# Kernel tuning notes

Measured on AMD Instinct MI355X. Metric: run time of the kernel, lower is better.

Reference implementation:

```python
import jax, jax.numpy as jnp
import numpy as np

SEQ_LEN, BATCH, VOCAB, EMB, HID, LAYERS = 128, 64, 10000, 1024, 1024, 2

def setup_inputs() -> dict:
    key = jax.random.key(0)
    ks = jax.random.split(key, 8)
    inputs = jax.random.randint(ks[0], (SEQ_LEN, BATCH), 0, VOCAB)
    hidden = jnp.zeros((LAYERS, BATCH, HID), jnp.float32)
    # parameters (uniform init like the torch module)
    emb = jax.random.uniform(ks[1], (VOCAB, EMB), jnp.float32, -0.1, 0.1)
    # per-layer RNN cell params (emb_size == hidden_size so Wx stacks uniformly)
    s = 1.0 / np.sqrt(HID)
    Wx = jax.random.uniform(ks[2], (LAYERS, HID, HID), jnp.float32, -s, s)
    Wh = jax.random.uniform(ks[3], (LAYERS, HID, HID), jnp.float32, -s, s)
    b = jax.random.uniform(ks[4], (LAYERS, HID), jnp.float32, -s, s)
    fcW = jax.random.uniform(ks[5], (VOCAB, HID), jnp.float32, -0.1, 0.1)
    fcb = jnp.zeros((VOCAB,), jnp.float32)
    return {"inputs": inputs, "hidden": hidden, "emb": emb, "Wx": Wx,
            "Wh": Wh, "b": b, "fcW": fcW, "fcb": fcb}

def reference(inputs, hidden, emb, Wx, Wh, b, fcW, fcb):
    num_layers = hidden.shape[0]

    def step(h, tok):
        x = emb[tok]  # [B, EMB] embedding lookup (dropout = identity, keep_prob=1)
        new_h = []
        for j in range(num_layers):  # small static loop over layers
            hj = jnp.tanh(x @ Wx[j] + h[j] @ Wh[j] + b[j])  # [B, H]
            new_h.append(hj)
            x = hj
        logits = x @ fcW.T + fcb  # [B, V]
        return jnp.stack(new_h), logits

    h_final, logits = jax.lax.scan(step, hidden, inputs)
    return logits, h_final  # [S,B,V], [L,B,H]
```

## Files before the change

kernel.cpp:

```cpp
#include <hip/hip_runtime.h>
#include <hip/hip_bf16.h>
#include <math.h>

typedef __hip_bfloat16 bf16;
typedef __attribute__((ext_vector_type(8))) short short8;
typedef __attribute__((ext_vector_type(4))) float floatx4;

#define SEQ   128
#define BATCH 64
#define VOCAB 10000
#define HID   1024
#define TAIL  81920000

#define MFMA(a,b,c) __builtin_amdgcn_mfma_f32_16x16x32_bf16((a),(b),(c),0,0,0)

__device__ inline void gl_lds16(const bf16* g, bf16* s) {
  __builtin_amdgcn_global_load_lds(
      (const __attribute__((address_space(1))) void*)g,
      (__attribute__((address_space(3))) void*)s, 16, 0, 0);
}

__device__ inline float ld_in(const void* p, size_t i, int f) {
  return f ? ((const float*)p)[i] : __bfloat162float(((const bf16*)p)[i]);
}

__global__ __launch_bounds__(256) void detect(const unsigned short* __restrict__ u,
                                              int* __restrict__ flag) {
  __shared__ int smax;
  if (threadIdx.x == 0) smax = 0;
  __syncthreads();
  int mymax = 0;
  for (int i = threadIdx.x * 2; i < 4096; i += 512) {
    int e = (u[i] >> 7) & 0xFF;
    mymax = max(mymax, e);
  }
  atomicMax(&smax, mymax);
  __syncthreads();
  if (threadIdx.x == 0) {
    flag[0] = (smax >= 0xF0) ? 1 : 0;
    flag[1] = 0;
  }
}

__global__ __launch_bounds__(256) void convert_any(const void* __restrict__ src,
                                                   bf16* __restrict__ dst, int n,
                                                   const int* __restrict__ flagp) {
  int f = *flagp;
  for (int i = blockIdx.x * 256 + threadIdx.x; i < n; i += gridDim.x * 256)
    dst[i] = __float2bfloat16(ld_in(src, (size_t)i, f));
}

__global__ __launch_bounds__(256) void transpose4(const void* __restrict__ Wx,
                                                  const void* __restrict__ Wh,
                                                  bf16* __restrict__ Wt,
                                                  const int* __restrict__ flagp) {
  __shared__ bf16 tile[64][65];
  int f = *flagp;
  int z = blockIdx.z;
  const void* src = (z & 1) ? Wh : Wx;
  size_t loff = (z >> 1) ? (size_t)HID * HID : 0;
  bf16* dst = Wt + (size_t)z * HID * HID;
  int r0 = blockIdx.x * 64, c0 = blockIdx.y * 64;
  int t = threadIdx.x, cc = t & 63, rg = t >> 6;
  #pragma unroll
  for (int i = 0; i < 16; ++i) {
    int r = rg * 16 + i;
    tile[r][cc] = __float2bfloat16(ld_in(src, loff + (size_t)(r0 + r) * HID + c0 + cc, f));
  }
  __syncthreads();
  #pragma unroll
  for (int i = 0; i < 16; ++i) {
    int j = rg * 16 + i;
    dst[(size_t)(c0 + j) * HID + r0 + cc] = tile[cc][j];
  }
}

__global__ __launch_bounds__(256) void gemm_a0(
    const int*  __restrict__ tok,
    const bf16* __restrict__ emb,
    const bf16* __restrict__ Wx0t,
    const bf16* __restrict__ b0,
    float* __restrict__ A0)
{
  __shared__ __align__(16) bf16 sA[128 * 32];
  __shared__ __align__(16) bf16 sB[128 * 32];
  int m0 = blockIdx.x * 128, n0 = blockIdx.y * 128;
  int t = threadIdx.x, lane = t & 63, w = t >> 6;
  int wm = (w >> 1) * 64, wn = (w & 1) * 64;
  int quad = lane >> 4, l16 = lane & 15;

  int r0 = t >> 2, kc = t & 3;
  const bf16* ga0 = emb + (size_t)tok[m0 + r0] * HID + kc * 8;
  const bf16* ga1 = emb + (size_t)tok[m0 + r0 + 64] * HID + kc * 8;
  const bf16* gb0 = Wx0t + (size_t)(n0 + r0) * HID + kc * 8;
  const bf16* gb1 = gb0 + (size_t)64 * HID;
  bf16* sa0 = sA + t * 8;  bf16* sa1 = sA + (t + 256) * 8;
  bf16* sb0 = sB + t * 8;  bf16* sb1 = sB + (t + 256) * 8;

  floatx4 acc[4][4];
  #pragma unroll
  for (int j = 0; j < 4; ++j) {
    float bv = __bfloat162float(b0[n0 + wn + j * 16 + l16]);
    #pragma unroll
    for (int i = 0; i < 4; ++i) acc[i][j] = (floatx4){bv, bv, bv, bv};
  }

  for (int kt = 0; kt < 32; ++kt) {
    gl_lds16(ga0, sa0); gl_lds16(ga1, sa1);
    gl_lds16(gb0, sb0); gl_lds16(gb1, sb1);
    ga0 += 32; ga1 += 32; gb0 += 32; gb1 += 32;
    __syncthreads();
    short8 af[4], bfr[4];
    #pragma unroll
    for (int i = 0; i < 4; ++i)
      af[i] = *(const short8*)(sA + (wm + i * 16 + l16) * 32 + quad * 8);
    #pragma unroll
    for (int j = 0; j < 4; ++j)
      bfr[j] = *(const short8*)(sB + (wn + j * 16 + l16) * 32 + quad * 8);
    #pragma unroll
    for (int i = 0; i < 4; ++i)
      #pragma unroll
      for (int j = 0; j < 4; ++j)
        acc[i][j] = MFMA(af[i], bfr[j], acc[i][j]);
    __syncthreads();
  }

  #pragma unroll
  for (int i = 0; i < 4; ++i)
    #pragma unroll
    for (int j = 0; j < 4; ++j)
      #pragma unroll
      for (int r = 0; r < 4; ++r) {
        int row = wm + i * 16 + quad * 4 + r;
        int col = wn + j * 16 + l16;
        A0[(size_t)(m0 + row) * HID + n0 + col] = acc[i][j][r];
      }
}

__device__ inline void gridbar(int* cnt, int expect) {
  __syncthreads();
  if (threadIdx.x == 0) {
    __threadfence();
    __hip_atomic_fetch_add(cnt, 1, __ATOMIC_RELEASE, __HIP_MEMORY_SCOPE_AGENT);
    while (__hip_atomic_load(cnt, __ATOMIC_ACQUIRE, __HIP_MEMORY_SCOPE_AGENT) < expect)
      __builtin_amdgcn_s_sleep(1);
    __threadfence();
  }
  __syncthreads();
}

__global__ __launch_bounds__(256) void wavefront_persist(
    const float* __restrict__ A0,
    const bf16* __restrict__ Wt,
    const bf16* __restrict__ bvecB,
    const bf16* __restrict__ hidB,
    bf16* __restrict__ h0a, bf16* __restrict__ h0b,
    bf16* __restrict__ h1a, bf16* __restrict__ h1b,
    bf16* __restrict__ H1hist,
    void* __restrict__ outv,
    int* __restrict__ flagp)
{
  __shared__ short8 sW8[4096];
  char* sWb = (char*)sW8;
  const int f = flagp[0];
  int* bar = flagp + 1;
  const int blk = blockIdx.x;
  const int t = threadIdx.x, lane = t & 63, w = t >> 6;
  const int quad = lane >> 4, l16 = lane & 15;
  const int m = w * 16;
  const bool isH1 = blk >= 32;

  const bf16* Wh0t = Wt + (size_t)1 * HID * HID;
  const bf16* Wx1t = Wt + (size_t)2 * HID * HID;
  const bf16* Wh1t = Wt + (size_t)3 * HID * HID;

  if (!isH1) {
    const int n0 = blk * 32;
    #pragma unroll
    for (int i = 0; i < 16; ++i) {
      int idx = i * 256 + t;
      int row = idx >> 7, c16 = idx & 127;
      short8 v = *(const short8*)(Wh0t + (size_t)(n0 + row) * HID + c16 * 8);
      int off = (c16 >> 2) * 2048 + (row >> 4) * 1024 + (c16 & 3) * 256 + (row & 15) * 16;
      *(short8*)(sWb + off) = v;
    }
  } else {
    const int n0 = (blk - 32) * 16;
    #pragma unroll
    for (int i = 0; i < 8; ++i) {
      int idx = i * 256 + t;
      int row = idx >> 7, c16 = idx & 127;
      int off = (c16 >> 2) * 1024 + (c16 & 3) * 256 + (row & 15) * 16;
      *(short8*)(sWb + off)         = *(const short8*)(Wx1t + (size_t)(n0 + row) * HID + c16 * 8);
      *(short8*)(sWb + 32768 + off) = *(const short8*)(Wh1t + (size_t)(n0 + row) * HID + c16 * 8);
    }
  }
  __syncthreads();

  for (int k = 0; k <= 128; ++k) {
    if (!isH1) {
      if (k <= 127) {
        const int n0 = blk * 32;
        const bf16* hp = (k == 0) ? hidB : ((k & 1) ? h0a : h0b);
        const bf16* aB = hp + (size_t)(m + l16) * HID + quad * 8;
        const char* b0p = sWb + lane * 16;
        const char* b1p = sWb + 1024 + lane * 16;
        floatx4 acc[2] = {};
        #pragma unroll 8
        for (int kt = 0; kt < 32; ++kt) {
          short8 a = *(const short8*)(aB + kt * 32);
          acc[0] = MFMA(a, *(const short8*)(b0p + kt * 2048), acc[0]);
          acc[1] = MFMA(a, *(const short8*)(b1p + kt * 2048), acc[1]);
        }
        bf16* hw = (k & 1) ? h0b : h0a;
        #pragma unroll
        for (int j = 0; j < 2; ++j)
          #pragma unroll
          for (int r = 0; r < 4; ++r) {
            int row = m + quad * 4 + r, col = n0 + j * 16 + l16;
            float pre = acc[j][r] + A0[(size_t)(k * 64 + row) * HID + col];
            float v = tanhf(pre);
            bf16 bv = __float2bfloat16(v);
            hw[row * HID + col] = bv;
            if (k == 127) {
              size_t o = (size_t)TAIL + row * HID + col;
              if (f) ((float*)outv)[o] = v; else ((bf16*)outv)[o] = bv;
            }
          }
      }
    } else {
      if (k >= 1) {
        const int n0 = (blk - 32) * 16;
        const bf16* a1p = (k & 1) ? h0a : h0b;
        const bf16* a2p = (k == 1) ? (hidB + 64 * HID)
                                   : ((k & 1) ? h1a : h1b);
        const bf16* aB1 = a1p + (size_t)(m + l16) * HID + quad * 8;
        const bf16* aB2 = a2p + (size_t)(m + l16) * HID + quad * 8;
        const char* bXp = sWb + lane * 16;
        const char* bHp = sWb + 32768 + lane * 16;
        floatx4 accX = {}, accH = {};
        #pragma unroll 8
        for (int kt = 0; kt < 32; ++kt) {
          short8 a = *(const short8*)(aB1 + kt * 32);
          accX = MFMA(a, *(const short8*)(bXp + kt * 1024), accX);
          short8 c = *(const short8*)(aB2 + kt * 32);
          accH = MFMA(c, *(const short8*)(bHp + kt * 1024), accH);
        }
        bf16* hw = (k & 1) ? h1b : h1a;
        #pragma unroll
        for (int r = 0; r < 4; ++r) {
          int row = m + quad * 4 + r, col = n0 + l16;
          float v = tanhf(accX[r] + accH[r] + __bfloat162float(bvecB[HID + col]));
          bf16 bv = __float2bfloat16(v);
          hw[row * HID + col] = bv;
          H1hist[(size_t)((k - 1) * 64 + row) * HID + col] = bv;
          if (k == 128) {
            size_t o = (size_t)TAIL + 64 * HID + row * HID + col;
            if (f) ((float*)outv)[o] = v; else ((bf16*)outv)[o] = bv;
          }
        }
      }
    }
    if (k < 128) gridbar(bar, (k + 1) * 96);
  }
}

__global__ __launch_bounds__(256) void gemm_logits(
    const bf16* __restrict__ H1,
    const bf16* __restrict__ fcW,
    const bf16* __restrict__ fcb,
    void* __restrict__ outv,
    const int* __restrict__ flagp)
{
  __shared__ __align__(16) bf16 sA[128 * 32];
  __shared__ __align__(16) bf16 sB[128 * 32];
  int f = *flagp;
  int m0 = blockIdx.x * 128, n0 = blockIdx.y * 128;
  int t = threadIdx.x, lane = t & 63, w = t >> 6;
  int wm = (w >> 1) * 64, wn = (w & 1) * 64;
  int quad = lane >> 4, l16 = lane & 15;

  int r0 = t >> 2, kc = t & 3;
  int rB0 = n0 + r0;      if (rB0 > VOCAB - 1) rB0 = VOCAB - 1;
  int rB1 = n0 + r0 + 64; if (rB1 > VOCAB - 1) rB1 = VOCAB - 1;
  const bf16* ga0 = H1 + (size_t)(m0 + r0) * HID + kc * 8;
  const bf16* ga1 = ga0 + (size_t)64 * HID;
  const bf16* gb0 = fcW + (size_t)rB0 * HID + kc * 8;
  const bf16* gb1 = fcW + (size_t)rB1 * HID + kc * 8;
  bf16* sa0 = sA + t * 8;  bf16* sa1 = sA + (t + 256) * 8;
  bf16* sb0 = sB + t * 8;  bf16* sb1 = sB + (t + 256) * 8;

  floatx4 acc[4][4];
  #pragma unroll
  for (int j = 0; j < 4; ++j) {
    int c = n0 + wn + j * 16 + l16;
    float bv = __bfloat162float(fcb[c > VOCAB - 1 ? VOCAB - 1 : c]);
    #pragma unroll
    for (int i = 0; i < 4; ++i) acc[i][j] = (floatx4){bv, bv, bv, bv};
  }

  for (int kt = 0; kt < 32; ++kt) {
    gl_lds16(ga0, sa0); gl_lds16(ga1, sa1);
    gl_lds16(gb0, sb0); gl_lds16(gb1, sb1);
    ga0 += 32; ga1 += 32; gb0 += 32; gb1 += 32;
    __syncthreads();
    short8 af[4], bfr[4];
    #pragma unroll
    for (int i = 0; i < 4; ++i)
      af[i] = *(const short8*)(sA + (wm + i * 16 + l16) * 32 + quad * 8);
    #pragma unroll
    for (int j = 0; j < 4; ++j)
      bfr[j] = *(const short8*)(sB + (wn + j * 16 + l16) * 32 + quad * 8);
    #pragma unroll
    for (int i = 0; i < 4; ++i)
      #pragma unroll
      for (int j = 0; j < 4; ++j)
        acc[i][j] = MFMA(af[i], bfr[j], acc[i][j]);
    __syncthreads();
  }

  #pragma unroll
  for (int i = 0; i < 4; ++i)
    #pragma unroll
    for (int j = 0; j < 4; ++j)
      #pragma unroll
      for (int r = 0; r < 4; ++r) {
        int row = wm + i * 16 + quad * 4 + r;
        int col = n0 + wn + j * 16 + l16;
        if (col < VOCAB) {
          size_t o = (size_t)(m0 + row) * VOCAB + col;
          if (f) ((float*)outv)[o] = acc[i][j][r];
          else   ((bf16*)outv)[o] = __float2bfloat16(acc[i][j][r]);
        }
      }
}

extern "C" void kernel_launch(void* const* d_in, const int* in_sizes, int n_in,
                              void* d_out, int out_size, void* d_ws, size_t ws_size,
                              hipStream_t stream)
{
  const int*  tok     = (const int*)d_in[0];
  const void* hid_raw = d_in[1];
  const void* emb_raw = d_in[2];
  const void* Wx_raw  = d_in[3];
  const void* Wh_raw  = d_in[4];
  const void* b_raw   = d_in[5];
  const void* fcW_raw = d_in[6];
  const void* fcb_raw = d_in[7];

  char* ws = (char*)d_ws;
  float* A0   = (float*)ws;
  bf16*  Wt   = (bf16*)(ws + 33554432);
  bf16*  H1   = (bf16*)(ws + 41943040);
  bf16*  h0a  = (bf16*)(ws + 58720256);
  bf16*  h0b  = h0a + 65536;
  bf16*  h1a  = h0b + 65536;
  bf16*  h1b  = h1a + 65536;
  bf16*  embB = (bf16*)(ws + 59244544);
  bf16*  fcwB = (bf16*)(ws + 79724544);
  bf16*  bvecB= (bf16*)(ws + 100204544);
  bf16*  fcbB = (bf16*)(ws + 100208640);
  bf16*  hidB = (bf16*)(ws + 100228640);
  int*   flag = (int*)(ws + 100490784);

  detect<<<1, 256, 0, stream>>>((const unsigned short*)emb_raw, flag);
  convert_any<<<2048, 256, 0, stream>>>(emb_raw, embB, VOCAB * HID, flag);
  convert_any<<<2048, 256, 0, stream>>>(fcW_raw, fcwB, VOCAB * HID, flag);
  convert_any<<<8,    256, 0, stream>>>(b_raw,   bvecB, 2 * HID, flag);
  convert_any<<<40,   256, 0, stream>>>(fcb_raw, fcbB, VOCAB, flag);
  convert_any<<<512,  256, 0, stream>>>(hid_raw, hidB, 2 * BATCH * HID, flag);
  transpose4<<<dim3(16, 16, 4), 256, 0, stream>>>(Wx_raw, Wh_raw, Wt, flag);
  gemm_a0<<<dim3(64, 8), 256, 0, stream>>>(tok, embB, Wt, bvecB, A0);
  wavefront_persist<<<96, 256, 0, stream>>>(A0, Wt, bvecB, hidB,
                                            h0a, h0b, h1a, h1b, H1, d_out, flag);
  gemm_logits<<<dim3(64, 79), 256, 0, stream>>>(H1, fcwB, fcbB, d_out, flag);
}
```

Baseline: 2.882 ms.

## Replace global grid barrier with per-layer counters and ring-buffered hidden states

Removes the all-block grid barrier in the persistent recurrence kernel and replaces it with two progress counters, one per layer. Layer-0 blocks can run up to 32 steps ahead of layer-1 by using a 32-slot ring of hidden-state panels, while layer 1 uses a 3-slot ring. Hidden values are packed in pairs and written with relaxed atomic stores, and all A-operand loads for a step are issued before the MFMAs. The emb and fcW conversions now share one workspace buffer, with the fcW conversion moved after gemm_a0. The aim is to cut synchronisation stalls and let the two layers overlap, at the cost of more complex producer/consumer ordering that could race if the counters or ring depths are wrong.

```diff
diff --git a/kernel.cpp b/kernel.cpp
--- a/kernel.cpp
+++ b/kernel.cpp
@@ -11,8 +11,22 @@
 #define VOCAB 10000
 #define HID   1024
 #define TAIL  81920000
+#define PNL   131072
 
 #define MFMA(a,b,c) __builtin_amdgcn_mfma_f32_16x16x32_bf16((a),(b),(c),0,0,0)
+
+#define LDA_U64(p)   __hip_atomic_load((const unsigned long long*)(p), __ATOMIC_RELAXED, __HIP_MEMORY_SCOPE_AGENT)
+#define LDAQ_I32(p)  __hip_atomic_load((const int*)(p), __ATOMIC_ACQUIRE, __HIP_MEMORY_SCOPE_AGENT)
+#define STA_U32(p,v) __hip_atomic_store((unsigned int*)(p), (v), __ATOMIC_RELAXED, __HIP_MEMORY_SCOPE_AGENT)
+#define ADDR_I32(p)  __hip_atomic_fetch_add((int*)(p), 1, __ATOMIC_RELEASE, __HIP_MEMORY_SCOPE_AGENT)
+
+union U16B { unsigned long long u[2]; short8 s; };
+
+__device__ inline unsigned int pack2(float lo, float hi) {
+  unsigned short a = __builtin_bit_cast(unsigned short, __float2bfloat16(lo));
+  unsigned short b = __builtin_bit_cast(unsigned short, __float2bfloat16(hi));
+  return ((unsigned int)b << 16) | (unsigned int)a;
+}
 
 __device__ inline void gl_lds16(const bf16* g, bf16* s) {
   __builtin_amdgcn_global_load_lds(
@@ -39,6 +53,7 @@
   if (threadIdx.x == 0) {
     flag[0] = (smax >= 0xF0) ? 1 : 0;
     flag[1] = 0;
+    flag[2] = 0;
   }
 }
 
@@ -48,6 +63,18 @@
   int f = *flagp;
   for (int i = blockIdx.x * 256 + threadIdx.x; i < n; i += gridDim.x * 256)
     dst[i] = __float2bfloat16(ld_in(src, (size_t)i, f));
+}
+
+__global__ __launch_bounds__(256) void init_hidden(const void* __restrict__ src,
+                                                   bf16* __restrict__ h0,
+                                                   bf16* __restrict__ h1,
+                                                   const int* __restrict__ flagp) {
+  int f = *flagp;
+  int i = blockIdx.x * 256 + threadIdx.x;
+  if (i < 65536) {
+    h0[i] = __float2bfloat16(ld_in(src, (size_t)i, f));
+    h1[i] = __float2bfloat16(ld_in(src, (size_t)(65536 + i), f));
+  }
 }
 
 __global__ __launch_bounds__(256) void transpose4(const void* __restrict__ Wx,
@@ -137,25 +164,12 @@
       }
 }
 
-__device__ inline void gridbar(int* cnt, int expect) {
-  __syncthreads();
-  if (threadIdx.x == 0) {
-    __threadfence();
-    __hip_atomic_fetch_add(cnt, 1, __ATOMIC_RELEASE, __HIP_MEMORY_SCOPE_AGENT);
-    while (__hip_atomic_load(cnt, __ATOMIC_ACQUIRE, __HIP_MEMORY_SCOPE_AGENT) < expect)
-      __builtin_amdgcn_s_sleep(1);
-    __threadfence();
-  }
-  __syncthreads();
-}
-
 __global__ __launch_bounds__(256) void wavefront_persist(
     const float* __restrict__ A0,
     const bf16* __restrict__ Wt,
     const bf16* __restrict__ bvecB,
-    const bf16* __restrict__ hidB,
-    bf16* __restrict__ h0a, bf16* __restrict__ h0b,
-    bf16* __restrict__ h1a, bf16* __restrict__ h1b,
+    char* __restrict__ H0f,
+    char* __restrict__ H1f,
     bf16* __restrict__ H1hist,
     void* __restrict__ outv,
     int* __restrict__ flagp)
@@ -163,7 +177,9 @@
   __shared__ short8 sW8[4096];
   char* sWb = (char*)sW8;
   const int f = flagp[0];
-  int* bar = flagp + 1;
+  int* c0 = flagp + 1;
+  int* c1 = flagp + 2;
+  char* H1B = (char*)H1hist;
   const int blk = blockIdx.x;
   const int t = threadIdx.x, lane = t & 63, w = t >> 6;
   const int quad = lane >> 4, l16 = lane & 15;
@@ -197,71 +213,113 @@
   }
   __syncthreads();
 
-  for (int k = 0; k <= 128; ++k) {
-    if (!isH1) {
-      if (k <= 127) {
-        const int n0 = blk * 32;
-        const bf16* hp = (k == 0) ? hidB : ((k & 1) ? h0a : h0b);
-        const bf16* aB = hp + (size_t)(m + l16) * HID + quad * 8;
-        const char* b0p = sWb + lane * 16;
-        const char* b1p = sWb + 1024 + lane * 16;
-        floatx4 acc[2] = {};
-        #pragma unroll 8
-        for (int kt = 0; kt < 32; ++kt) {
-          short8 a = *(const short8*)(aB + kt * 32);
-          acc[0] = MFMA(a, *(const short8*)(b0p + kt * 2048), acc[0]);
-          acc[1] = MFMA(a, *(const short8*)(b1p + kt * 2048), acc[1]);
-        }
-        bf16* hw = (k & 1) ? h0b : h0a;
+  if (!isH1) {
+    const int n0 = blk * 32;
+    const char* b0p = sWb + lane * 16;
+    const char* b1p = sWb + 1024 + lane * 16;
+    for (int k = 0; k < 128; ++k) {
+      if (t == 0) {
+        if (k > 0)   while (LDAQ_I32(c0) < 32 * k)        __builtin_amdgcn_s_sleep(1);
+        if (k >= 32) while (LDAQ_I32(c1) < 64 * (k - 31)) __builtin_amdgcn_s_sleep(1);
+      }
+      __syncthreads();
+
+      const char* aB = H0f + (size_t)(k & 31) * PNL + (m + l16) * 2048 + quad * 16;
+      U16B a[32];
+      #pragma unroll
+      for (int kt = 0; kt < 32; ++kt) {
+        a[kt].u[0] = LDA_U64(aB + kt * 64);
+        a[kt].u[1] = LDA_U64(aB + kt * 64 + 8);
+      }
+      float a0r[2][4];
+      #pragma unroll
+      for (int j = 0; j < 2; ++j)
         #pragma unroll
-        for (int j = 0; j < 2; ++j)
-          #pragma unroll
-          for (int r = 0; r < 4; ++r) {
-            int row = m + quad * 4 + r, col = n0 + j * 16 + l16;
-            float pre = acc[j][r] + A0[(size_t)(k * 64 + row) * HID + col];
-            float v = tanhf(pre);
-            bf16 bv = __float2bfloat16(v);
-            hw[row * HID + col] = bv;
-            if (k == 127) {
-              size_t o = (size_t)TAIL + row * HID + col;
-              if (f) ((float*)outv)[o] = v; else ((bf16*)outv)[o] = bv;
-            }
-          }
-      }
-    } else {
-      if (k >= 1) {
-        const int n0 = (blk - 32) * 16;
-        const bf16* a1p = (k & 1) ? h0a : h0b;
-        const bf16* a2p = (k == 1) ? (hidB + 64 * HID)
-                                   : ((k & 1) ? h1a : h1b);
-        const bf16* aB1 = a1p + (size_t)(m + l16) * HID + quad * 8;
-        const bf16* aB2 = a2p + (size_t)(m + l16) * HID + quad * 8;
-        const char* bXp = sWb + lane * 16;
-        const char* bHp = sWb + 32768 + lane * 16;
-        floatx4 accX = {}, accH = {};
-        #pragma unroll 8
-        for (int kt = 0; kt < 32; ++kt) {
-          short8 a = *(const short8*)(aB1 + kt * 32);
-          accX = MFMA(a, *(const short8*)(bXp + kt * 1024), accX);
-          short8 c = *(const short8*)(aB2 + kt * 32);
-          accH = MFMA(c, *(const short8*)(bHp + kt * 1024), accH);
-        }
-        bf16* hw = (k & 1) ? h1b : h1a;
+        for (int r = 0; r < 4; ++r)
+          a0r[j][r] = A0[(size_t)(k * 64 + m + quad * 4 + r) * HID + n0 + j * 16 + l16];
+
+      floatx4 acc0 = {}, acc1 = {};
+      #pragma unroll
+      for (int kt = 0; kt < 32; ++kt) {
+        acc0 = MFMA(a[kt].s, *(const short8*)(b0p + kt * 2048), acc0);
+        acc1 = MFMA(a[kt].s, *(const short8*)(b1p + kt * 2048), acc1);
+      }
+
+      char* wp = H0f + (size_t)((k + 1) & 31) * PNL;
+      #pragma unroll
+      for (int j = 0; j < 2; ++j) {
+        floatx4 ac = j ? acc1 : acc0;
         #pragma unroll
         for (int r = 0; r < 4; ++r) {
-          int row = m + quad * 4 + r, col = n0 + l16;
-          float v = tanhf(accX[r] + accH[r] + __bfloat162float(bvecB[HID + col]));
-          bf16 bv = __float2bfloat16(v);
-          hw[row * HID + col] = bv;
-          H1hist[(size_t)((k - 1) * 64 + row) * HID + col] = bv;
-          if (k == 128) {
-            size_t o = (size_t)TAIL + 64 * HID + row * HID + col;
-            if (f) ((float*)outv)[o] = v; else ((bf16*)outv)[o] = bv;
+          int row = m + quad * 4 + r, col = n0 + j * 16 + l16;
+          float v = tanhf(ac[r] + a0r[j][r]);
+          float pv = __shfl_xor(v, 1);
+          if (k == 127) {
+            size_t o = (size_t)TAIL + (size_t)row * HID + col;
+            if (f) ((float*)outv)[o] = v;
+            else   ((bf16*)outv)[o] = __float2bfloat16(v);
           }
-        }
-      }
+          if (!(l16 & 1))
+            STA_U32(wp + row * 2048 + col * 2, pack2(v, pv));
+        }
+      }
+      __syncthreads();
+      if (t == 0) ADDR_I32(c0);
     }
-    if (k < 128) gridbar(bar, (k + 1) * 96);
+  } else {
+    const int n0 = (blk - 32) * 16;
+    const char* bXp = sWb + lane * 16;
+    const char* bHp = sWb + 32768 + lane * 16;
+    const float bb = __bfloat162float(bvecB[HID + n0 + l16]);
+    for (int s = 0; s < 128; ++s) {
+      if (t == 0) {
+        while (LDAQ_I32(c0) < 32 * (s + 1)) __builtin_amdgcn_s_sleep(1);
+        if (s > 0) while (LDAQ_I32(c1) < 64 * s) __builtin_amdgcn_s_sleep(1);
+      }
+      __syncthreads();
+
+      const char* aX = H0f + (size_t)((s + 1) & 31) * PNL + (m + l16) * 2048 + quad * 16;
+      const char* aH = H1f + (size_t)(s % 3) * PNL + (m + l16) * 2048 + quad * 16;
+      floatx4 accX = {}, accH = {};
+      #pragma unroll
+      for (int half = 0; half < 2; ++half) {
+        U16B x[16], h[16];
+        #pragma unroll
+        for (int i = 0; i < 16; ++i) {
+          int kt = half * 16 + i;
+          x[i].u[0] = LDA_U64(aX + kt * 64);
+          x[i].u[1] = LDA_U64(aX + kt * 64 + 8);
+          h[i].u[0] = LDA_U64(aH + kt * 64);
+          h[i].u[1] = LDA_U64(aH + kt * 64 + 8);
+        }
+        #pragma unroll
+        for (int i = 0; i < 16; ++i) {
+          int kt = half * 16 + i;
+          accX = MFMA(x[i].s, *(const short8*)(bXp + kt * 1024), accX);
+          accH = MFMA(h[i].s, *(const short8*)(bHp + kt * 1024), accH);
+        }
+      }
+
+      char* wp = H1f + (size_t)((s + 1) % 3) * PNL;
+      #pragma unroll
+      for (int r = 0; r < 4; ++r) {
+        int row = m + quad * 4 + r, col = n0 + l16;
+        float v = tanhf(accX[r] + accH[r] + bb);
+        float pv = __shfl_xor(v, 1);
+        if (s == 127) {
+          size_t o = (size_t)TAIL + 64 * HID + (size_t)row * HID + col;
+          if (f) ((float*)outv)[o] = v;
+          else   ((bf16*)outv)[o] = __float2bfloat16(v);
+        }
+        if (!(l16 & 1)) {
+          unsigned int pk = pack2(v, pv);
+          STA_U32(wp + row * 2048 + col * 2, pk);
+          STA_U32(H1B + ((size_t)(s * 64 + row) * HID + col) * 2, pk);
+        }
+      }
+      __syncthreads();
+      if (t == 0) ADDR_I32(c1);
+    }
   }
 }
 
@@ -349,29 +407,25 @@
   const void* fcb_raw = d_in[7];
 
   char* ws = (char*)d_ws;
-  float* A0   = (float*)ws;
-  bf16*  Wt   = (bf16*)(ws + 33554432);
-  bf16*  H1   = (bf16*)(ws + 41943040);
-  bf16*  h0a  = (bf16*)(ws + 58720256);
-  bf16*  h0b  = h0a + 65536;
-  bf16*  h1a  = h0b + 65536;
-  bf16*  h1b  = h1a + 65536;
-  bf16*  embB = (bf16*)(ws + 59244544);
-  bf16*  fcwB = (bf16*)(ws + 79724544);
-  bf16*  bvecB= (bf16*)(ws + 100204544);
-  bf16*  fcbB = (bf16*)(ws + 100208640);
-  bf16*  hidB = (bf16*)(ws + 100228640);
-  int*   flag = (int*)(ws + 100490784);
+  float* A0    = (float*)ws;
+  bf16*  Wt    = (bf16*)(ws + 33554432);
+  bf16*  H1hist= (bf16*)(ws + 41943040);
+  char*  H0f   = ws + 58720256;
+  char*  H1f   = ws + 62914560;
+  bf16*  shared= (bf16*)(ws + 63307776);
+  bf16*  bvecB = (bf16*)(ws + 83787776);
+  bf16*  fcbB  = (bf16*)(ws + 83791872);
+  int*   flag  = (int*)(ws + 83811872);
 
   detect<<<1, 256, 0, stream>>>((const unsigned short*)emb_raw, flag);
-  convert_any<<<2048, 256, 0, stream>>>(emb_raw, embB, VOCAB * HID, flag);
-  convert_any<<<2048, 256, 0, stream>>>(fcW_raw, fcwB, VOCAB * HID, flag);
+  convert_any<<<2048, 256, 0, stream>>>(emb_raw, shared, VOCAB * HID, flag);
   convert_any<<<8,    256, 0, stream>>>(b_raw,   bvecB, 2 * HID, flag);
   convert_any<<<40,   256, 0, stream>>>(fcb_raw, fcbB, VOCAB, flag);
-  convert_any<<<512,  256, 0, stream>>>(hid_raw, hidB, 2 * BATCH * HID, flag);
+  init_hidden<<<256, 256, 0, stream>>>(hid_raw, (bf16*)H0f, (bf16*)H1f, flag);
   transpose4<<<dim3(16, 16, 4), 256, 0, stream>>>(Wx_raw, Wh_raw, Wt, flag);
-  gemm_a0<<<dim3(64, 8), 256, 0, stream>>>(tok, embB, Wt, bvecB, A0);
-  wavefront_persist<<<96, 256, 0, stream>>>(A0, Wt, bvecB, hidB,
-                                            h0a, h0b, h1a, h1b, H1, d_out, flag);
-  gemm_logits<<<dim3(64, 79), 256, 0, stream>>>(H1, fcwB, fcbB, d_out, flag);
-}
+  gemm_a0<<<dim3(64, 8), 256, 0, stream>>>(tok, shared, Wt, bvecB, A0);
+  convert_any<<<2048, 256, 0, stream>>>(fcW_raw, shared, VOCAB * HID, flag);
+  wavefront_persist<<<96, 256, 0, stream>>>(A0, Wt, bvecB, H0f, H1f,
+                                            H1hist, d_out, flag);
+  gemm_logits<<<dim3(64, 79), 256, 0, stream>>>(H1hist, shared, fcbB, d_out, flag);
+}
```

Result: slower. 3.028 ms (+5.0%).
